# Performance work log

Hardware: AMD Instinct MI355X
Metric: run time of the kernel (lower is better)

Reference implementation:

```python
import jax, jax.numpy as jnp
import numpy as np

B, N, H = 4, 256, 8            # batch, nodes, heads
DNI, DEI = 32, 16              # node_in_dim, edge_in_dim
DNO, DEO = 32, 32              # node_out_dim, edge_out_dim
LEAKY = 0.2
NEG = -9e15


def setup_inputs() -> dict:
    key = jax.random.key(0)
    ks = jax.random.split(key, 13)
    s = 0.05
    node_fea = jax.random.normal(ks[0], (B, H, N, DNI), jnp.float32)
    edge_fea = jax.random.normal(ks[1], (B, H, N, N, DEI), jnp.float32)
    adj = jax.random.randint(ks[2], (B, N, N), 0, 2, jnp.int32)
    # learned params (nn.Linear: y = x @ W.T + b)
    W_w   = jax.random.normal(ks[3],  (H * DNO, H * DNI), jnp.float32) * s
    W_b   = jax.random.normal(ks[4],  (H * DNO,),         jnp.float32) * s
    a1_w  = jax.random.normal(ks[5],  (H, H * DNO),       jnp.float32) * s
    a2_w  = jax.random.normal(ks[6],  (H, H * DNO),       jnp.float32) * s
    ae_w  = jax.random.normal(ks[7],  (H, H * DEI),       jnp.float32) * s
    ae_b  = jax.random.normal(ks[8],  (H,),               jnp.float32) * s
    We_w  = jax.random.normal(ks[9],  (H * DEO, H * DEI), jnp.float32) * s
    We_b  = jax.random.normal(ks[10], (H * DEO,),         jnp.float32) * s
    Wod_w = jax.random.normal(ks[11], (H * DNO, H * DNI), jnp.float32) * s
    Wod_b = jax.random.normal(ks[12], (H * DNO,),         jnp.float32) * s
    return dict(node_fea=node_fea, edge_fea=edge_fea, adj=adj,
                W_w=W_w, W_b=W_b, a1_w=a1_w, a2_w=a2_w,
                ae_w=ae_w, ae_b=ae_b, We_w=We_w, We_b=We_b,
                Wod_w=Wod_w, Wod_b=Wod_b)


def reference(node_fea, edge_fea, adj, W_w, W_b, a1_w, a2_w,
              ae_w, ae_b, We_w, We_b, Wod_w, Wod_b):
    b, h, n, _ = node_fea.shape  # h == nheads -> non-first-layer branch
    # flatten heads into feature dim, as in the torch code
    nf = node_fea.transpose(0, 2, 1, 3).reshape(b, n, -1)          # [B,N,H*DNI]
    ef = edge_fea.transpose(0, 2, 3, 1, 4).reshape(b, n, n, -1)    # [B,N,N,H*DEI]

    Wh = nf @ W_w.T + W_b                                          # [B,N,H*DNO]
    e_edge = ef @ ae_w.T + ae_b                                    # [B,N,N,H]
    Whi = Wh @ a1_w.T                                              # [B,N,H]
    Whj = Wh @ a2_w.T                                              # [B,N,H]

    e = Whi[:, :, None, :] + Whj[:, None, :, :] + e_edge           # [B,N,N,H]
    e = jax.nn.leaky_relu(e, LEAKY)
    e = jnp.where(adj[..., None] > 0, e, NEG)

    # edge update: o + d + W_edge(edge)
    od = nf @ Wod_w.T + Wod_b                                      # [B,N,H*DEO]
    edge_new = od[:, :, None, :] + od[:, None, :, :] + (ef @ We_w.T + We_b)
    edge_new = edge_new.reshape(b, n, n, h, -1).transpose(0, 3, 1, 2, 4)  # [B,H,N,N,DEO]

    att = jax.nn.softmax(e.transpose(0, 3, 1, 2), axis=-1)         # [B,H,N,N]; dropout p=0 -> identity
    Whh = Wh.reshape(b, n, h, -1).transpose(0, 2, 1, 3)            # [B,H,N,DNO]
    node_new = att @ Whh + Whh                                     # [B,H,N,DNO]
    return node_new, edge_new
```

## Files before the change

### kernel.cpp

```cpp
#include <hip/hip_runtime.h>
#include <cstddef>


typedef __attribute__((ext_vector_type(8))) short short8;
typedef __attribute__((ext_vector_type(4))) float f32x4;

__device__ __forceinline__ float bf2f(unsigned short u) {
  union { unsigned int i; float f; } c;
  c.i = ((unsigned int)u) << 16;
  return c.f;
}
__device__ __forceinline__ unsigned short f2bf(float f) {
  union { float f; unsigned int i; } c; c.f = f;
  unsigned int x = c.i;
  x += 0x7fffu + ((x >> 16) & 1u);
  return (unsigned short)(x >> 16);
}

struct F8 { f32x4 lo, hi; };

__device__ __forceinline__ float loadf(const void* p, size_t i, bool bf) {
  return bf ? bf2f(((const unsigned short*)p)[i]) : ((const float*)p)[i];
}
__device__ __forceinline__ F8 load8f(const void* p, size_t i, bool bf) {
  F8 r;
  if (bf) {
    short8 s = *(const short8*)((const unsigned short*)p + i);
    #pragma unroll
    for (int k = 0; k < 4; k++) {
      r.lo[k] = bf2f((unsigned short)s[k]);
      r.hi[k] = bf2f((unsigned short)s[k + 4]);
    }
  } else {
    const float* f = (const float*)p + i;
    r.lo = *(const f32x4*)f;
    r.hi = *(const f32x4*)(f + 4);
  }
  return r;
}
__device__ __forceinline__ short8 load8bf(const void* p, size_t i, bool bf) {
  if (bf) return *(const short8*)((const unsigned short*)p + i);
  const float* f = (const float*)p + i;
  f32x4 a = *(const f32x4*)f, c = *(const f32x4*)(f + 4);
  short8 r;
  #pragma unroll
  for (int k = 0; k < 4; k++) {
    r[k]     = (short)f2bf(a[k]);
    r[k + 4] = (short)f2bf(c[k]);
  }
  return r;
}
__device__ __forceinline__ void storef(void* p, size_t i, float v, bool bf) {
  if (bf) ((unsigned short*)p)[i] = f2bf(v);
  else    ((float*)p)[i] = v;
}

__global__ void k_detect(const unsigned int* __restrict__ w, int* __restrict__ flag) {
  const int lane = threadIdx.x;
  unsigned int x = w[lane];
  unsigned int e = (x >> 7) & 0xFFu;
  bool hit = (e >= 100u && e <= 126u);
  unsigned long long b = __ballot(hit);
  if (lane == 0) *flag = (__popcll(b) >= 32) ? 1 : 0;
}

__global__ __launch_bounds__(256) void k_node(
    const void* __restrict__ node_fea,
    const void* __restrict__ W_w,  const void* __restrict__ W_b,
    const void* __restrict__ a1_w, const void* __restrict__ a2_w,
    const void* __restrict__ Wod_w, const void* __restrict__ Wod_b,
    const int* __restrict__ flag,
    float* __restrict__ wh, float* __restrict__ od,
    float* __restrict__ whi, float* __restrict__ whj)
{
  const bool bf = (*flag != 0);
  __shared__ float nf[2][256];
  __shared__ float red[4][32];
  const int t = threadIdx.x;
  const int row0 = blockIdx.x * 2;
  const int b = row0 >> 8;
  {
    const int rl = t >> 7, k2 = (t & 127) * 2;
    const int h = k2 >> 5, d = k2 & 31;
    const int n = (row0 & 255) + rl;
    const size_t idx = (((size_t)(b * 8 + h)) * 256 + n) * 32 + d;
    nf[rl][k2]     = loadf(node_fea, idx, bf);
    nf[rl][k2 + 1] = loadf(node_fea, idx + 1, bf);
  }
  __syncthreads();
  const int o = t;
  float acc1[2] = {0.f, 0.f}, acc2[2] = {0.f, 0.f};
  #pragma unroll 4
  for (int kc = 0; kc < 32; kc++) {
    F8 w1 = load8f(W_w,   (size_t)o * 256 + kc * 8, bf);
    F8 w2 = load8f(Wod_w, (size_t)o * 256 + kc * 8, bf);
    #pragma unroll
    for (int r = 0; r < 2; r++) {
      f32x4 alo = *(const f32x4*)&nf[r][kc * 8];
      f32x4 ahi = *(const f32x4*)&nf[r][kc * 8 + 4];
      #pragma unroll
      for (int k = 0; k < 4; k++) {
        acc1[r] += alo[k] * w1.lo[k] + ahi[k] * w1.hi[k];
        acc2[r] += alo[k] * w2.lo[k] + ahi[k] * w2.hi[k];
      }
    }
  }
  float whv[2], odv[2];
  {
    float b1 = loadf(W_b, o, bf), b2 = loadf(Wod_b, o, bf);
    #pragma unroll
    for (int r = 0; r < 2; r++) {
      whv[r] = acc1[r] + b1;
      odv[r] = acc2[r] + b2;
      wh[(size_t)(row0 + r) * 256 + o] = whv[r];
      od[(size_t)(row0 + r) * 256 + o] = odv[r];
    }
  }
  float a1f[8], a2f[8];
  #pragma unroll
  for (int h = 0; h < 8; h++) {
    a1f[h] = loadf(a1_w, (size_t)h * 256 + o, bf);
    a2f[h] = loadf(a2_w, (size_t)h * 256 + o, bf);
  }
  const int lane = t & 63, wv = t >> 6;
  #pragma unroll 1
  for (int c = 0; c < 32; c++) {
    const int mat = c >> 4, r = (c >> 3) & 1, h = c & 7;
    float v = whv[r] * (mat ? a2f[h] : a1f[h]);
    #pragma unroll
    for (int s = 1; s < 64; s <<= 1) v += __shfl_xor(v, s, 64);
    if (lane == 0) red[wv][c] = v;
  }
  __syncthreads();
  if (t < 32) {
    const int c = t;
    float s = red[0][c] + red[1][c] + red[2][c] + red[3][c];
    const int mat = c >> 4, r = (c >> 3) & 1, h = c & 7;
    (mat ? whj : whi)[(size_t)(row0 + r) * 8 + h] = s;
  }
}

__global__ __launch_bounds__(256) void k_main(
    const void* __restrict__ edge_fea, const int* __restrict__ adj,
    const void* __restrict__ ae_w, const void* __restrict__ ae_b,
    const void* __restrict__ We_w, const void* __restrict__ We_b,
    const int* __restrict__ flag,
    const float* __restrict__ od, const float* __restrict__ whi,
    const float* __restrict__ whj, const float* __restrict__ wh,
    void* __restrict__ out)
{
  const bool bf = (*flag != 0);
  __shared__ unsigned short A[128][136];
  __shared__ float e_l[8][256];
  const int t = threadIdx.x;
  const int blk = blockIdx.x;
  const int i = blk & 255, b = blk >> 8;
  const int wave = t >> 6, lane = t & 63, quad = lane >> 4, col = lane & 15;

  short8 bw[4][4];
  #pragma unroll
  for (int s = 0; s < 4; s++) {
    const int n = (wave * 4 + s) * 16 + col;
    #pragma unroll
    for (int ks = 0; ks < 4; ks++)
      bw[s][ks] = load8bf(We_w, (size_t)n * 128 + ks * 32 + quad * 8, bf);
  }
  short8 bae[4];
  #pragma unroll
  for (int ks = 0; ks < 4; ks++) {
    short8 z = {0, 0, 0, 0, 0, 0, 0, 0};
    bae[ks] = (col < 8) ? load8bf(ae_w, (size_t)col * 128 + ks * 32 + quad * 8, bf) : z;
  }

  float odi[4], web[4];
  #pragma unroll
  for (int s = 0; s < 4; s++) {
    const int f = (wave * 4 + s) * 16 + col;
    odi[s] = od[((size_t)(b * 256 + i)) * 256 + f];
    web[s] = loadf(We_b, f, bf);
  }
  float whi_h = 0.f, aeb = 0.f;
  if (col < 8) {
    whi_h = whi[(size_t)(b * 256 + i) * 8 + col];
    aeb   = loadf(ae_b, col, bf);
  }

  #pragma unroll 1
  for (int jt = 0; jt < 2; jt++) {
    const int j0 = jt * 128;
    {
      const int jr = t >> 1, e8 = (t & 1) * 8;
      #pragma unroll
      for (int h = 0; h < 8; h++) {
        const size_t idx = ((((size_t)(b * 8 + h)) * 256 + i) * 256 + j0 + jr) * 16 + e8;
        *(short8*)&A[jr][h * 16 + e8] = load8bf(edge_fea, idx, bf);
      }
    }
    __syncthreads();

    #pragma unroll 1
    for (int mt = 0; mt < 8; mt++) {
      f32x4 acc[4];
      f32x4 acce = {0.f, 0.f, 0.f, 0.f};
      #pragma unroll
      for (int s = 0; s < 4; s++) acc[s] = (f32x4){0.f, 0.f, 0.f, 0.f};
      const bool own = ((mt & 3) == wave);

      #pragma unroll
      for (int ks = 0; ks < 4; ks++) {
        short8 a = *(const short8*)&A[mt * 16 + col][ks * 32 + quad * 8];
        acc[0] = __builtin_amdgcn_mfma_f32_16x16x32_bf16(a, bw[0][ks], acc[0], 0, 0, 0);
        acc[1] = __builtin_amdgcn_mfma_f32_16x16x32_bf16(a, bw[1][ks], acc[1], 0, 0, 0);
        acc[2] = __builtin_amdgcn_mfma_f32_16x16x32_bf16(a, bw[2][ks], acc[2], 0, 0, 0);
        acc[3] = __builtin_amdgcn_mfma_f32_16x16x32_bf16(a, bw[3][ks], acc[3], 0, 0, 0);
        if (own) acce = __builtin_amdgcn_mfma_f32_16x16x32_bf16(a, bae[ks], acce, 0, 0, 0);
      }

      const int jb = j0 + mt * 16 + quad * 4;
      #pragma unroll
      for (int s = 0; s < 4; s++) {
        const int nt = wave * 4 + s;
        const int h = nt >> 1, d = (nt & 1) * 16 + col;
        const size_t obase =
            262144 + ((((size_t)(b * 8 + h)) * 256 + i) * 256 + jb) * 32 + d;
        const float* odp = od + ((size_t)(b * 256) + jb) * 256 + nt * 16 + col;
        #pragma unroll
        for (int r = 0; r < 4; r++) {
          float v = acc[s][r] + odi[s] + web[s] + odp[(size_t)r * 256];
          storef(out, obase + (size_t)r * 32, v, bf);
        }
      }
      if (own && col < 8) {
        #pragma unroll
        for (int r = 0; r < 4; r++) {
          const int jj = jb + r;
          float e = acce[r] + aeb + whi_h + whj[(size_t)(b * 256 + jj) * 8 + col];
          e = (e > 0.f) ? e : 0.2f * e;
          e = (adj[(size_t)(b * 256 + i) * 256 + jj] > 0) ? e : -9e15f;
          e_l[col][jj] = e;
        }
      }
    }
    __syncthreads();
  }

  {
    const int h = t >> 5, l32 = t & 31;
    float m = -3.0e38f;
    #pragma unroll
    for (int k = 0; k < 8; k++) m = fmaxf(m, e_l[h][l32 + 32 * k]);
    #pragma unroll
    for (int s = 16; s >= 1; s >>= 1) m = fmaxf(m, __shfl_xor(m, s, 32));
    float p[8], sum = 0.f;
    #pragma unroll
    for (int k = 0; k < 8; k++) {
      p[k] = __expf(e_l[h][l32 + 32 * k] - m);
      sum += p[k];
    }
    #pragma unroll
    for (int s = 16; s >= 1; s >>= 1) sum += __shfl_xor(sum, s, 32);
    const float inv = 1.0f / sum;
    #pragma unroll
    for (int k = 0; k < 8; k++) e_l[h][l32 + 32 * k] = p[k] * inv;
  }
  __syncthreads();

  {
    const int h = t >> 5;
    const float* whb = wh + ((size_t)b * 256) * 256;
    float acc = 0.f;
    #pragma unroll 4
    for (int j = 0; j < 256; j++) acc += e_l[h][j] * whb[(size_t)j * 256 + t];
    float v = acc + whb[(size_t)i * 256 + t];
    const size_t oe = (((size_t)(b * 8 + h)) * 256 + i) * 32 + (t & 31);
    storef(out, oe, v, bf);
  }
}

extern "C" void kernel_launch(void* const* d_in, const int* in_sizes, int n_in,
                              void* d_out, int out_size, void* d_ws, size_t ws_size,
                              hipStream_t stream) {
  const void* node_fea = d_in[0];
  const void* edge_fea = d_in[1];
  const int*  adj      = (const int*)d_in[2];
  const void* W_w      = d_in[3];
  const void* W_b      = d_in[4];
  const void* a1_w     = d_in[5];
  const void* a2_w     = d_in[6];
  const void* ae_w     = d_in[7];
  const void* ae_b     = d_in[8];
  const void* We_w     = d_in[9];
  const void* We_b     = d_in[10];
  const void* Wod_w    = d_in[11];
  const void* Wod_b    = d_in[12];

  int*   flag = (int*)d_ws;
  float* base = (float*)d_ws;
  float* wh   = base + 16;
  float* od   = wh + 262144;
  float* whi  = od + 262144;
  float* whj  = whi + 8192;

  k_detect<<<dim3(1), dim3(64), 0, stream>>>((const unsigned int*)W_w, flag);
  k_node<<<dim3(512), dim3(256), 0, stream>>>(node_fea, W_w, W_b, a1_w, a2_w,
                                              Wod_w, Wod_b, flag, wh, od, whi, whj);
  k_main<<<dim3(1024), dim3(256), 0, stream>>>(edge_fea, adj, ae_w, ae_b, We_w, We_b,
                                               flag, od, whi, whj, wh, d_out);
}
```

Baseline: 597.2 us.

## Swizzle LDS tile, swap MFMA operands for vector stores, transpose Wh for attention

Replaces the padded LDS edge tile with an XOR-swizzled layout. It swaps the MFMA operand order so each lane holds four consecutive output features, which enables 16-byte nontemporal output stores and vectorized od loads. The attention-logit MFMA moves out of the main loop into a separate pass split across waves. Wh is stored transposed so the final att@Wh product reads contiguous float4 rows, and launch bounds request 4 blocks per CU. The aim is fewer scalar strided global accesses and fewer LDS bank conflicts, at the cost of more register pressure and an extra pass over the LDS tile.

Result: faster. 561.5 us (-6.0%).

```diff
diff --git a/kernel.cpp b/kernel.cpp
--- a/kernel.cpp
+++ b/kernel.cpp
@@ -3,6 +3,7 @@
 
 
 typedef __attribute__((ext_vector_type(8))) short short8;
+typedef __attribute__((ext_vector_type(4))) short short4v;
 typedef __attribute__((ext_vector_type(4))) float f32x4;
 
 __device__ __forceinline__ float bf2f(unsigned short u) {
@@ -21,6 +22,16 @@
 
 __device__ __forceinline__ float loadf(const void* p, size_t i, bool bf) {
   return bf ? bf2f(((const unsigned short*)p)[i]) : ((const float*)p)[i];
+}
+__device__ __forceinline__ f32x4 load4f(const void* p, size_t i, bool bf) {
+  f32x4 r;
+  if (bf) {
+    #pragma unroll
+    for (int k = 0; k < 4; k++) r[k] = bf2f(((const unsigned short*)p)[i + k]);
+  } else {
+    r = *(const f32x4*)((const float*)p + i);
+  }
+  return r;
 }
 __device__ __forceinline__ F8 load8f(const void* p, size_t i, bool bf) {
   F8 r;
@@ -70,7 +81,7 @@
     const void* __restrict__ a1_w, const void* __restrict__ a2_w,
     const void* __restrict__ Wod_w, const void* __restrict__ Wod_b,
     const int* __restrict__ flag,
-    float* __restrict__ wh, float* __restrict__ od,
+    float* __restrict__ whT, float* __restrict__ od,
     float* __restrict__ whi, float* __restrict__ whj)
 {
   const bool bf = (*flag != 0);
@@ -112,7 +123,7 @@
     for (int r = 0; r < 2; r++) {
       whv[r] = acc1[r] + b1;
       odv[r] = acc2[r] + b2;
-      wh[(size_t)(row0 + r) * 256 + o] = whv[r];
+      whT[(((size_t)(b * 256 + o)) << 8) + (row0 & 255) + r] = whv[r];
       od[(size_t)(row0 + r) * 256 + o] = odv[r];
     }
   }
@@ -140,17 +151,17 @@
   }
 }
 
-__global__ __launch_bounds__(256) void k_main(
+__global__ __launch_bounds__(256, 4) void k_main(
     const void* __restrict__ edge_fea, const int* __restrict__ adj,
     const void* __restrict__ ae_w, const void* __restrict__ ae_b,
     const void* __restrict__ We_w, const void* __restrict__ We_b,
     const int* __restrict__ flag,
     const float* __restrict__ od, const float* __restrict__ whi,
-    const float* __restrict__ whj, const float* __restrict__ wh,
+    const float* __restrict__ whj, const float* __restrict__ whT,
     void* __restrict__ out)
 {
   const bool bf = (*flag != 0);
-  __shared__ unsigned short A[128][136];
+  __shared__ unsigned short A[16384];
   __shared__ float e_l[8][256];
   const int t = threadIdx.x;
   const int blk = blockIdx.x;
@@ -165,24 +176,14 @@
     for (int ks = 0; ks < 4; ks++)
       bw[s][ks] = load8bf(We_w, (size_t)n * 128 + ks * 32 + quad * 8, bf);
   }
-  short8 bae[4];
-  #pragma unroll
-  for (int ks = 0; ks < 4; ks++) {
-    short8 z = {0, 0, 0, 0, 0, 0, 0, 0};
-    bae[ks] = (col < 8) ? load8bf(ae_w, (size_t)col * 128 + ks * 32 + quad * 8, bf) : z;
-  }
-
-  float odi[4], web[4];
+
+  f32x4 ow4[4];
   #pragma unroll
   for (int s = 0; s < 4; s++) {
-    const int f = (wave * 4 + s) * 16 + col;
-    odi[s] = od[((size_t)(b * 256 + i)) * 256 + f];
-    web[s] = loadf(We_b, f, bf);
-  }
-  float whi_h = 0.f, aeb = 0.f;
-  if (col < 8) {
-    whi_h = whi[(size_t)(b * 256 + i) * 8 + col];
-    aeb   = loadf(ae_b, col, bf);
+    const int f0 = (wave * 4 + s) * 16 + quad * 4;
+    f32x4 oi = *(const f32x4*)(od + (((size_t)(b * 256 + i)) << 8) + f0);
+    f32x4 wb = load4f(We_b, f0, bf);
+    ow4[s] = oi + wb;
   }
 
   #pragma unroll 1
@@ -190,54 +191,89 @@
     const int j0 = jt * 128;
     {
       const int jr = t >> 1, e8 = (t & 1) * 8;
+      unsigned short* arow = &A[jr * 128];
+      const int sx = jr & 7;
       #pragma unroll
       for (int h = 0; h < 8; h++) {
         const size_t idx = ((((size_t)(b * 8 + h)) * 256 + i) * 256 + j0 + jr) * 16 + e8;
-        *(short8*)&A[jr][h * 16 + e8] = load8bf(edge_fea, idx, bf);
+        const int slot = (h * 2 + (e8 >> 3)) ^ sx;
+        *(short8*)(arow + slot * 8) = load8bf(edge_fea, idx, bf);
       }
     }
     __syncthreads();
 
     #pragma unroll 1
     for (int mt = 0; mt < 8; mt++) {
+      const int row = mt * 16 + col;
+      const unsigned short* arow = &A[row * 128];
+      const int rx = row & 7;
       f32x4 acc[4];
-      f32x4 acce = {0.f, 0.f, 0.f, 0.f};
       #pragma unroll
       for (int s = 0; s < 4; s++) acc[s] = (f32x4){0.f, 0.f, 0.f, 0.f};
-      const bool own = ((mt & 3) == wave);
-
       #pragma unroll
       for (int ks = 0; ks < 4; ks++) {
-        short8 a = *(const short8*)&A[mt * 16 + col][ks * 32 + quad * 8];
-        acc[0] = __builtin_amdgcn_mfma_f32_16x16x32_bf16(a, bw[0][ks], acc[0], 0, 0, 0);
-        acc[1] = __builtin_amdgcn_mfma_f32_16x16x32_bf16(a, bw[1][ks], acc[1], 0, 0, 0);
-        acc[2] = __builtin_amdgcn_mfma_f32_16x16x32_bf16(a, bw[2][ks], acc[2], 0, 0, 0);
-        acc[3] = __builtin_amdgcn_mfma_f32_16x16x32_bf16(a, bw[3][ks], acc[3], 0, 0, 0);
-        if (own) acce = __builtin_amdgcn_mfma_f32_16x16x32_bf16(a, bae[ks], acce, 0, 0, 0);
-      }
-
-      const int jb = j0 + mt * 16 + quad * 4;
+        short8 a = *(const short8*)(arow + ((ks * 4 + quad) ^ rx) * 8);
+        acc[0] = __builtin_amdgcn_mfma_f32_16x16x32_bf16(bw[0][ks], a, acc[0], 0, 0, 0);
+        acc[1] = __builtin_amdgcn_mfma_f32_16x16x32_bf16(bw[1][ks], a, acc[1], 0, 0, 0);
+        acc[2] = __builtin_amdgcn_mfma_f32_16x16x32_bf16(bw[2][ks], a, acc[2], 0, 0, 0);
+        acc[3] = __builtin_amdgcn_mfma_f32_16x16x32_bf16(bw[3][ks], a, acc[3], 0, 0, 0);
+      }
+      const int j = j0 + mt * 16 + col;
+      const float* odj = od + (((size_t)(b * 256 + j)) << 8);
       #pragma unroll
       for (int s = 0; s < 4; s++) {
-        const int nt = wave * 4 + s;
-        const int h = nt >> 1, d = (nt & 1) * 16 + col;
-        const size_t obase =
-            262144 + ((((size_t)(b * 8 + h)) * 256 + i) * 256 + jb) * 32 + d;
-        const float* odp = od + ((size_t)(b * 256) + jb) * 256 + nt * 16 + col;
+        const int f0 = (wave * 4 + s) * 16 + quad * 4;
+        const int h = f0 >> 5, d0 = f0 & 31;
+        f32x4 op = *(const f32x4*)(odj + f0);
+        f32x4 v = acc[s] + ow4[s] + op;
+        const size_t oidx =
+            262144 + (((((size_t)(b * 8 + h)) * 256 + i) * 256 + j) * 32 + d0);
+        if (bf) {
+          short4v sv;
+          #pragma unroll
+          for (int r = 0; r < 4; r++) sv[r] = (short)f2bf(v[r]);
+          __builtin_nontemporal_store(sv, (short4v*)((unsigned short*)out + oidx));
+        } else {
+          __builtin_nontemporal_store(v, (f32x4*)((float*)out + oidx));
+        }
+      }
+    }
+
+    {
+      short8 bae[4];
+      #pragma unroll
+      for (int ks = 0; ks < 4; ks++) {
+        short8 z = {0, 0, 0, 0, 0, 0, 0, 0};
+        bae[ks] = (col < 8) ? load8bf(ae_w, (size_t)col * 128 + ks * 32 + quad * 8, bf) : z;
+      }
+      f32x4 whi4 = {0.f, 0.f, 0.f, 0.f}, aeb4 = {0.f, 0.f, 0.f, 0.f};
+      if (quad < 2) {
+        whi4 = *(const f32x4*)(whi + ((size_t)(b * 256 + i)) * 8 + quad * 4);
+        aeb4 = load4f(ae_b, quad * 4, bf);
+      }
+      #pragma unroll
+      for (int mm = 0; mm < 2; mm++) {
+        const int mt = wave * 2 + mm;
+        const int row = mt * 16 + col;
+        const unsigned short* arow = &A[row * 128];
+        const int rx = row & 7;
+        f32x4 acce = {0.f, 0.f, 0.f, 0.f};
         #pragma unroll
-        for (int r = 0; r < 4; r++) {
-          float v = acc[s][r] + odi[s] + web[s] + odp[(size_t)r * 256];
-          storef(out, obase + (size_t)r * 32, v, bf);
+        for (int ks = 0; ks < 4; ks++) {
+          short8 a = *(const short8*)(arow + ((ks * 4 + quad) ^ rx) * 8);
+          acce = __builtin_amdgcn_mfma_f32_16x16x32_bf16(bae[ks], a, acce, 0, 0, 0);
         }
-      }
-      if (own && col < 8) {
-        #pragma unroll
-        for (int r = 0; r < 4; r++) {
-          const int jj = jb + r;
-          float e = acce[r] + aeb + whi_h + whj[(size_t)(b * 256 + jj) * 8 + col];
-          e = (e > 0.f) ? e : 0.2f * e;
-          e = (adj[(size_t)(b * 256 + i) * 256 + jj] > 0) ? e : -9e15f;
-          e_l[col][jj] = e;
+        if (quad < 2) {
+          const int j = j0 + mt * 16 + col;
+          f32x4 wj = *(const f32x4*)(whj + ((size_t)(b * 256 + j)) * 8 + quad * 4);
+          const int av = adj[((size_t)(b * 256 + i)) * 256 + j];
+          #pragma unroll
+          for (int r = 0; r < 4; r++) {
+            float e = acce[r] + aeb4[r] + whi4[r] + wj[r];
+            e = (e > 0.f) ? e : 0.2f * e;
+            e = (av > 0) ? e : -9e15f;
+            e_l[quad * 4 + r][j] = e;
+          }
         }
       }
     }
@@ -267,11 +303,15 @@
 
   {
     const int h = t >> 5;
-    const float* whb = wh + ((size_t)b * 256) * 256;
-    float acc = 0.f;
-    #pragma unroll 4
-    for (int j = 0; j < 256; j++) acc += e_l[h][j] * whb[(size_t)j * 256 + t];
-    float v = acc + whb[(size_t)i * 256 + t];
+    const float* wr = whT + (((size_t)(b * 256 + t)) << 8);
+    f32x4 a4 = {0.f, 0.f, 0.f, 0.f};
+    #pragma unroll 8
+    for (int j4 = 0; j4 < 64; j4++) {
+      f32x4 w4 = *(const f32x4*)(wr + j4 * 4);
+      const f32x4 p4 = *(const f32x4*)&e_l[h][j4 * 4];
+      a4 += w4 * p4;
+    }
+    float v = (a4[0] + a4[1]) + (a4[2] + a4[3]) + wr[i];
     const size_t oe = (((size_t)(b * 8 + h)) * 256 + i) * 32 + (t & 31);
     storef(out, oe, v, bf);
   }
@@ -296,14 +336,14 @@
 
   int*   flag = (int*)d_ws;
   float* base = (float*)d_ws;
-  float* wh   = base + 16;
-  float* od   = wh + 262144;
+  float* whT  = base + 16;
+  float* od   = whT + 262144;
   float* whi  = od + 262144;
   float* whj  = whi + 8192;
 
   k_detect<<<dim3(1), dim3(64), 0, stream>>>((const unsigned int*)W_w, flag);
   k_node<<<dim3(512), dim3(256), 0, stream>>>(node_fea, W_w, W_b, a1_w, a2_w,
-                                              Wod_w, Wod_b, flag, wh, od, whi, whj);
+                                              Wod_w, Wod_b, flag, whT, od, whi, whj);
   k_main<<<dim3(1024), dim3(256), 0, stream>>>(edge_fea, adj, ae_w, ae_b, We_w, We_b,
-                                               flag, od, whi, whj, wh, d_out);
-}
+                                               flag, od, whi, whj, whT, d_out);
+}
```
